# Kernel optimization log

Hardware: AMD Instinct MI355X
Metric: run time of the kernel (lower is better)

## Reference

```python
import jax, jax.numpy as jnp
import numpy as np
import math

B, T, D = 2, 2048, 2048
N_HEADS, N_KV_HEADS = 16, 4
HEAD_DIM = D // N_HEADS          # 128
N_GROUPS = N_HEADS // N_KV_HEADS # 4


def setup_inputs() -> dict:
    key = jax.random.key(0)
    k1, k2, k3, k4, k5 = jax.random.split(key, 5)
    x = jax.random.normal(k1, (B, T, D), dtype=jnp.float32)
    # RoPE table: [T, head_dim//2, 2] = (cos, sin)
    inv_freq = 1.0 / (10000.0 ** (np.arange(0, HEAD_DIM, 2, dtype=np.float32) / HEAD_DIM))
    ang = np.arange(T, dtype=np.float32)[:, None] * inv_freq[None, :]  # [T, hd/2]
    rope = jnp.asarray(np.stack([np.cos(ang), np.sin(ang)], axis=-1), dtype=jnp.float32)
    s = 0.02
    wq = s * jax.random.normal(k2, (N_HEADS * HEAD_DIM, D), dtype=jnp.float32)
    wk = s * jax.random.normal(k3, (N_KV_HEADS * HEAD_DIM, D), dtype=jnp.float32)
    wv = s * jax.random.normal(k4, (N_KV_HEADS * HEAD_DIM, D), dtype=jnp.float32)
    wo = s * jax.random.normal(k5, (D, D), dtype=jnp.float32)
    return {"x": x, "rope": rope, "wq": wq, "wk": wk, "wv": wv, "wo": wo}


def apply_rope(t, rope):
    # t: [B, H, T, hd]; rope: [T, hd/2, 2]
    d = t.shape[-1]
    t1, t2 = t[..., : d // 2], t[..., d // 2 :]
    cos = rope[..., 0][None, None]  # [1,1,T,hd/2]
    sin = rope[..., 1][None, None]
    return jnp.concatenate([t1 * cos - t2 * sin, t1 * sin + t2 * cos], axis=-1)


def reference(x, rope, wq, wk, wv, wo):
    b, t, c = x.shape
    q = (x @ wq.T).reshape(b, t, N_HEADS, HEAD_DIM).transpose(0, 2, 1, 3)
    k = (x @ wk.T).reshape(b, t, N_KV_HEADS, HEAD_DIM).transpose(0, 2, 1, 3)
    v = (x @ wv.T).reshape(b, t, N_KV_HEADS, HEAD_DIM).transpose(0, 2, 1, 3)
    q = apply_rope(q, rope)
    k = apply_rope(k, rope)
    k = jnp.repeat(k, N_GROUPS, axis=1)  # [B, H, T, hd]
    v = jnp.repeat(v, N_GROUPS, axis=1)
    scale = 1.0 / math.sqrt(HEAD_DIM)
    scores = jnp.einsum("bhqd,bhkd->bhqk", q, k) * scale
    causal = jnp.tril(jnp.ones((t, t), dtype=bool))
    scores = jnp.where(causal[None, None], scores, jnp.finfo(scores.dtype).min)
    attn = jax.nn.softmax(scores, axis=-1)
    y = jnp.einsum("bhqk,bhkd->bhqd", attn, v)
    y = y.transpose(0, 2, 1, 3).reshape(b, t, c)
    return y @ wo.T
```

## Files before the change

kernel.cpp:

```cpp
#include <hip/hip_runtime.h>

typedef unsigned short u16;
typedef float   f32x4  __attribute__((ext_vector_type(4)));
typedef short   short8 __attribute__((ext_vector_type(8)));
typedef __bf16  bf16x8 __attribute__((ext_vector_type(8)));
typedef float   float4v __attribute__((ext_vector_type(4)));
typedef unsigned short u16x4 __attribute__((ext_vector_type(4)));

static __device__ __forceinline__ u16 f2b(float f) {
  return __builtin_bit_cast(u16, (__bf16)f);
}
static __device__ __forceinline__ float b2f(u16 h) {
  union { unsigned u; float f; } v; v.u = ((unsigned)h) << 16;
  return v.f;
}
static __device__ __forceinline__ f32x4 mfma_bf16(short8 a, short8 b, f32x4 c) {
  return __builtin_amdgcn_mfma_f32_16x16x32_bf16(
      __builtin_bit_cast(bf16x8, a), __builtin_bit_cast(bf16x8, b), c, 0, 0, 0);
}
static __device__ __forceinline__ void gload_lds16(const u16* g, u16* l) {
  __builtin_amdgcn_global_load_lds(
      (const __attribute__((address_space(1))) unsigned int*)g,
      (__attribute__((address_space(3))) unsigned int*)l, 16, 0, 0);
}

#define BB 2
#define TT 2048
#define DD 2048
#define NH 16
#define NKVH 4
#define HD 128
#define MM (BB * TT)
#define QSTR 3072
#define QSCALE 0.08838834764831845f

#define N4_X   ((MM * DD) / 4)
#define N4_WQ  ((DD * DD) / 4)
#define N4_WKV ((NKVH * HD * DD) / 4)
#define N4_WO  ((DD * DD) / 4)
#define N4_TOT (N4_X + N4_WQ + 2 * N4_WKV + N4_WO)

__global__ __launch_bounds__(256) void cvt_all(const float* __restrict__ x,
                                               const float* __restrict__ wq,
                                               const float* __restrict__ wk,
                                               const float* __restrict__ wv,
                                               const float* __restrict__ wo,
                                               u16* __restrict__ xb,
                                               u16* __restrict__ wqkvb,
                                               u16* __restrict__ wob) {
  int stride = gridDim.x * blockDim.x;
  for (int i = blockIdx.x * blockDim.x + threadIdx.x; i < N4_TOT; i += stride) {
    const float4v* src;
    u16x4* dst;
    int off;
    if (i < N4_X) {
      src = (const float4v*)x; dst = (u16x4*)xb; off = i;
    } else if (i < N4_X + N4_WQ) {
      src = (const float4v*)wq; dst = (u16x4*)wqkvb; off = i - N4_X;
    } else if (i < N4_X + N4_WQ + N4_WKV) {
      src = (const float4v*)wk; dst = (u16x4*)wqkvb + N4_WQ; off = i - (N4_X + N4_WQ);
    } else if (i < N4_X + N4_WQ + 2 * N4_WKV) {
      src = (const float4v*)wv; dst = (u16x4*)wqkvb + N4_WQ + N4_WKV;
      off = i - (N4_X + N4_WQ + N4_WKV);
    } else {
      src = (const float4v*)wo; dst = (u16x4*)wob; off = i - (N4_X + N4_WQ + 2 * N4_WKV);
    }
    float4v v = src[off];
    u16x4 o;
    o[0] = f2b(v[0]); o[1] = f2b(v[1]); o[2] = f2b(v[2]); o[3] = f2b(v[3]);
    dst[off] = o;
  }
}

__global__ __launch_bounds__(256) void rope_k(u16* __restrict__ K,
                                              const float* __restrict__ rope) {
  int idx = blockIdx.x * 256 + threadIdx.x;
  int i  = idx & 63;
  int h  = (idx >> 6) & (NKVH - 1);
  int bt = idx >> 8;
  int t  = bt & (TT - 1);
  size_t base = (size_t)bt * QSTR + h * HD + i;
  float x1 = b2f(K[base]);
  float x2 = b2f(K[base + 64]);
  float c = rope[t * 128 + 2 * i];
  float s = rope[t * 128 + 2 * i + 1];
  K[base]      = f2b(x1 * c - x2 * s);
  K[base + 64] = f2b(x1 * s + x2 * c);
}

template <bool OUTBF>
__global__ __launch_bounds__(256) void gemm_bt(const u16* __restrict__ A,
                                               const u16* __restrict__ W,
                                               void* __restrict__ Cout,
                                               int M, int N, int K) {
  __shared__ __align__(16) u16 As[128 * 32];
  __shared__ __align__(16) u16 Ws[128 * 32];
  const int tid = threadIdx.x, lane = tid & 63, wid = tid >> 6;
  const int wr = wid >> 1, wc = wid & 1;
  const int gx = gridDim.x;
  const int lin = blockIdx.y * gx + blockIdx.x;
  const int cpx = (gx * gridDim.y) >> 3;
  const int swz = (lin & 7) * cpx + (lin >> 3);
  const int brow = (swz / gx) * 128, bcol = (swz % gx) * 128;
  const int l15 = lane & 15, lh = lane >> 4;

  const int c0 = wid * 64 + lane;
  const int c1 = c0 + 256;
  const u16* Ag0 = A + (size_t)(brow + (c0 >> 2)) * K + ((c0 & 3) << 3);
  const u16* Ag1 = A + (size_t)(brow + (c1 >> 2)) * K + ((c1 & 3) << 3);
  const u16* Wg0 = W + (size_t)(bcol + (c0 >> 2)) * K + ((c0 & 3) << 3);
  const u16* Wg1 = W + (size_t)(bcol + (c1 >> 2)) * K + ((c1 & 3) << 3);
  u16* lA0 = &As[(wid * 64) * 8];
  u16* lA1 = &As[(wid * 64 + 256) * 8];
  u16* lW0 = &Ws[(wid * 64) * 8];
  u16* lW1 = &Ws[(wid * 64 + 256) * 8];

  f32x4 acc[4][4];
#pragma unroll
  for (int m = 0; m < 4; ++m)
#pragma unroll
    for (int n = 0; n < 4; ++n) acc[m][n] = (f32x4)0.0f;

  for (int k0 = 0; k0 < K; k0 += 32) {
    __syncthreads();
    gload_lds16(Ag0 + k0, lA0);
    gload_lds16(Ag1 + k0, lA1);
    gload_lds16(Wg0 + k0, lW0);
    gload_lds16(Wg1 + k0, lW1);
    __syncthreads();
    short8 af[4], bfr[4];
#pragma unroll
    for (int m = 0; m < 4; ++m)
      af[m] = *(const short8*)&As[(wr * 64 + m * 16 + l15) * 32 + (lh << 3)];
#pragma unroll
    for (int n = 0; n < 4; ++n)
      bfr[n] = *(const short8*)&Ws[(wc * 64 + n * 16 + l15) * 32 + (lh << 3)];
#pragma unroll
    for (int m = 0; m < 4; ++m)
#pragma unroll
      for (int n = 0; n < 4; ++n)
        acc[m][n] = mfma_bf16(af[m], bfr[n], acc[m][n]);
  }

#pragma unroll
  for (int m = 0; m < 4; ++m)
#pragma unroll
    for (int n = 0; n < 4; ++n)
#pragma unroll
      for (int j = 0; j < 4; ++j) {
        int row = brow + wr * 64 + m * 16 + lh * 4 + j;
        int col = bcol + wc * 64 + n * 16 + l15;
        if (OUTBF)
          ((u16*)Cout)[(size_t)row * N + col] = f2b(acc[m][n][j]);
        else
          ((float*)Cout)[(size_t)row * N + col] = acc[m][n][j];
      }
}

#define QBLK 128
#define KVBLK 128

static __device__ __forceinline__ void attn_tile(
    const short8* qa, f32x4* o, f32x4& ol, float* mrow,
    int qrow0, int kv0,
    const u16* Ks, const unsigned* Vt32, u16* myP,
    int l15, int lh, short8 ones8) {
  if (kv0 > qrow0 + 15) return;

  f32x4 s[4];
#pragma unroll
  for (int nt = 0; nt < 4; ++nt) s[nt] = (f32x4)0.0f;
  __builtin_amdgcn_s_setprio(1);
#pragma unroll
  for (int nt = 0; nt < 4; ++nt)
#pragma unroll
    for (int kk = 0; kk < 4; ++kk) {
      short8 kb = *(const short8*)&Ks[(nt * 16 + l15) * 136 + kk * 32 + (lh << 3)];
      s[nt] = mfma_bf16(qa[kk], kb, s[nt]);
    }
  __builtin_amdgcn_s_setprio(0);

  const int qg = qrow0 + lh * 4;
#pragma unroll
  for (int j = 0; j < 4; ++j)
#pragma unroll
    for (int nt = 0; nt < 4; ++nt)
      if (kv0 + nt * 16 + l15 > qg + j) s[nt][j] = -1e30f;

  float mt[4];
#pragma unroll
  for (int j = 0; j < 4; ++j)
    mt[j] = fmaxf(fmaxf(s[0][j], s[1][j]), fmaxf(s[2][j], s[3][j]));
#pragma unroll
  for (int d = 1; d <= 8; d <<= 1)
#pragma unroll
    for (int j = 0; j < 4; ++j) mt[j] = fmaxf(mt[j], __shfl_xor(mt[j], d));

  float gmax = mt[0] - mrow[0];
#pragma unroll
  for (int j = 1; j < 4; ++j) gmax = fmaxf(gmax, mt[j] - mrow[j]);
  if (!__all(gmax <= 8.0f)) {
#pragma unroll
    for (int j = 0; j < 4; ++j) {
      float mn = fmaxf(mrow[j], mt[j]);
      float a = __expf(mrow[j] - mn);
      mrow[j] = mn;
      ol[j] *= a;
#pragma unroll
      for (int n = 0; n < 8; ++n) o[n][j] *= a;
    }
  }

  f32x4 p[4];
#pragma unroll
  for (int nt = 0; nt < 4; ++nt)
#pragma unroll
    for (int j = 0; j < 4; ++j) p[nt][j] = __expf(s[nt][j] - mrow[j]);

#pragma unroll
  for (int nt = 0; nt < 4; ++nt)
#pragma unroll
    for (int j = 0; j < 4; ++j)
      myP[(lh * 4 + j) * 72 + nt * 16 + l15] = f2b(p[nt][j]);

  __builtin_amdgcn_s_setprio(1);
#pragma unroll
  for (int c = 0; c < 2; ++c) {
    short8 pa = *(const short8*)&myP[l15 * 72 + c * 32 + (lh << 3)];
    ol = mfma_bf16(pa, ones8, ol);
#pragma unroll
    for (int nt2 = 0; nt2 < 8; ++nt2) {
      int d = nt2 * 16 + l15;
      int byteoff = (d * 144 + (c * 32 + lh * 8) * 2) ^ (((d >> 3) & 7) << 4);
      short8 vb = *(const short8*)((const char*)Vt32 + byteoff);
      o[nt2] = mfma_bf16(pa, vb, o[nt2]);
    }
  }
  __builtin_amdgcn_s_setprio(0);
}

__global__ __launch_bounds__(512) void attn_kernel(const u16* __restrict__ QKV,
                                                   const float* __restrict__ rope,
                                                   u16* __restrict__ Y) {
  __shared__ __align__(16) u16 Ks[2][64 * 136];
  __shared__ __align__(16) unsigned Vt32[2][128 * 36];
  __shared__ __align__(16) u16 Ps[8][16 * 72];

  const int tid = threadIdx.x, lane = tid & 63, wid = tid >> 6;
  const int l15 = lane & 15, lh = lane >> 4;
  const int bid = blockIdx.x;
  const int qpair = bid & 7;
  const int h = (bid >> 3) & 15;
  const int b = bid >> 7;
  const int kvh = h >> 2;
  const int qtA = qpair, qtB = 15 - qpair;
  const int rowA = qtA * QBLK + wid * 16;
  const int rowB = qtB * QBLK + wid * 16;

  const u16* Kb_ = QKV + (size_t)b * TT * QSTR + DD + kvh * HD;
  const u16* Vb_ = Kb_ + NKVH * HD;

  short8 ones8;
#pragma unroll
  for (int e = 0; e < 8; ++e) ones8[e] = (short)0x3F80;

  short8 qaA[4], qaB[4];
  {
    const u16* qA = QKV + (size_t)(b * TT + rowA + l15) * QSTR + h * HD + (lh << 3);
    const u16* qB = QKV + (size_t)(b * TT + rowB + l15) * QSTR + h * HD + (lh << 3);
#pragma unroll
    for (int kk = 0; kk < 4; ++kk) {
      qaA[kk] = *(const short8*)(qA + kk * 32);
      qaB[kk] = *(const short8*)(qB + kk * 32);
    }
  }
  {
    const float* rpA = rope + (size_t)(rowA + l15) * 128;
    const float* rpB = rope + (size_t)(rowB + l15) * 128;
#pragma unroll
    for (int kk = 0; kk < 2; ++kk)
#pragma unroll
      for (int e = 0; e < 8; ++e) {
        const int i2 = 2 * (kk * 32 + (lh << 3) + e);
        float c = rpA[i2], s = rpA[i2 + 1];
        float x1 = b2f((u16)qaA[kk][e]), x2 = b2f((u16)qaA[kk + 2][e]);
        qaA[kk][e]     = (short)f2b(QSCALE * (x1 * c - x2 * s));
        qaA[kk + 2][e] = (short)f2b(QSCALE * (x1 * s + x2 * c));
        float cb = rpB[i2], sb = rpB[i2 + 1];
        float y1 = b2f((u16)qaB[kk][e]), y2 = b2f((u16)qaB[kk + 2][e]);
        qaB[kk][e]     = (short)f2b(QSCALE * (y1 * cb - y2 * sb));
        qaB[kk + 2][e] = (short)f2b(QSCALE * (y1 * sb + y2 * cb));
      }
  }

  f32x4 oA[8], oB[8];
  f32x4 olA = (f32x4)0.0f, olB = (f32x4)0.0f;
  float mA[4], mB[4];
#pragma unroll
  for (int n = 0; n < 8; ++n) { oA[n] = (f32x4)0.0f; oB[n] = (f32x4)0.0f; }
#pragma unroll
  for (int j = 0; j < 4; ++j) { mA[j] = -1e30f; mB[j] = -1e30f; }

  const int kvend = (qtB + 1) * QBLK;

  short8 kreg[4], vreg[4];
  const int srow = tid >> 4;
  const int sc8 = (tid & 15) << 3;

  auto issue = [&](int kv0) {
    kreg[0] = *(const short8*)&Kb_[(size_t)(kv0 + srow) * QSTR + sc8];
    kreg[1] = *(const short8*)&Kb_[(size_t)(kv0 + 32 + srow) * QSTR + sc8];
    kreg[2] = *(const short8*)&Kb_[(size_t)(kv0 + 64 + srow) * QSTR + sc8];
    kreg[3] = *(const short8*)&Kb_[(size_t)(kv0 + 96 + srow) * QSTR + sc8];
    vreg[0] = *(const short8*)&Vb_[(size_t)(kv0 + 2 * srow) * QSTR + sc8];
    vreg[1] = *(const short8*)&Vb_[(size_t)(kv0 + 2 * srow + 1) * QSTR + sc8];
    vreg[2] = *(const short8*)&Vb_[(size_t)(kv0 + 64 + 2 * srow) * QSTR + sc8];
    vreg[3] = *(const short8*)&Vb_[(size_t)(kv0 + 64 + 2 * srow + 1) * QSTR + sc8];
  };

  issue(0);
  for (int kv0 = 0; kv0 < kvend; kv0 += KVBLK) {
    __syncthreads();
    *(short8*)&Ks[0][srow * 136 + sc8] = kreg[0];
    *(short8*)&Ks[0][(srow + 32) * 136 + sc8] = kreg[1];
    *(short8*)&Ks[1][srow * 136 + sc8] = kreg[2];
    *(short8*)&Ks[1][(srow + 32) * 136 + sc8] = kreg[3];
#pragma unroll
    for (int e = 0; e < 8; ++e) {
      int d = sc8 + e;
      unsigned pk0 = (unsigned)(u16)vreg[0][e] | ((unsigned)(u16)vreg[1][e] << 16);
      unsigned pk1 = (unsigned)(u16)vreg[2][e] | ((unsigned)(u16)vreg[3][e] << 16);
      int byteoff = (d * 144 + 4 * srow) ^ (((d >> 3) & 7) << 4);
      *(unsigned*)((char*)&Vt32[0][0] + byteoff) = pk0;
      *(unsigned*)((char*)&Vt32[1][0] + byteoff) = pk1;
    }
    __syncthreads();
    if (kv0 + KVBLK < kvend) issue(kv0 + KVBLK);

    attn_tile(qaA, oA, olA, mA, rowA, kv0,      &Ks[0][0], &Vt32[0][0], &Ps[wid][0], l15, lh, ones8);
    attn_tile(qaA, oA, olA, mA, rowA, kv0 + 64, &Ks[1][0], &Vt32[1][0], &Ps[wid][0], l15, lh, ones8);
    attn_tile(qaB, oB, olB, mB, rowB, kv0,      &Ks[0][0], &Vt32[0][0], &Ps[wid][0], l15, lh, ones8);
    attn_tile(qaB, oB, olB, mB, rowB, kv0 + 64, &Ks[1][0], &Vt32[1][0], &Ps[wid][0], l15, lh, ones8);
  }

  f32x4 invA, invB;
#pragma unroll
  for (int j = 0; j < 4; ++j) {
    invA[j] = __builtin_amdgcn_rcpf(olA[j]);
    invB[j] = __builtin_amdgcn_rcpf(olB[j]);
  }
#pragma unroll
  for (int nt = 0; nt < 8; ++nt)
#pragma unroll
    for (int j = 0; j < 4; ++j) {
      Y[(size_t)(b * TT + rowA + lh * 4 + j) * DD + h * HD + nt * 16 + l15] =
          f2b(oA[nt][j] * invA[j]);
      Y[(size_t)(b * TT + rowB + lh * 4 + j) * DD + h * HD + nt * 16 + l15] =
          f2b(oB[nt][j] * invB[j]);
    }
}

extern "C" void kernel_launch(void* const* d_in, const int* in_sizes, int n_in,
                              void* d_out, int out_size, void* d_ws, size_t ws_size,
                              hipStream_t stream) {
  const float* x    = (const float*)d_in[0];
  const float* rope = (const float*)d_in[1];
  const float* wq   = (const float*)d_in[2];
  const float* wk   = (const float*)d_in[3];
  const float* wv   = (const float*)d_in[4];
  const float* wo   = (const float*)d_in[5];
  float* out = (float*)d_out;

  char* ws = (char*)d_ws;
  u16* xb    = (u16*)ws; ws += (size_t)MM * DD * 2;
  u16* wqkvb = (u16*)ws; ws += (size_t)QSTR * DD * 2;
  u16* wob   = (u16*)ws; ws += (size_t)DD * DD * 2;
  u16* QKVb  = (u16*)ws; ws += (size_t)MM * QSTR * 2;
  u16* Yb    = (u16*)ws;

  cvt_all<<<2048, 256, 0, stream>>>(x, wq, wk, wv, wo, xb, wqkvb, wob);

  gemm_bt<true><<<dim3(QSTR / 128, MM / 128), 256, 0, stream>>>(xb, wqkvb, QKVb, MM, QSTR, DD);

  rope_k<<<(MM * NKVH * 64) / 256, 256, 0, stream>>>(QKVb + DD, rope);

  attn_kernel<<<BB * NH * (TT / QBLK / 2), 512, 0, stream>>>(QKVb, rope, Yb);

  gemm_bt<false><<<dim3(DD / 128, MM / 128), 256, 0, stream>>>(Yb, wob, out, MM, DD, DD);
}
```

Baseline: 226.6 us.

## Add large-tile double-buffered QKV projection GEMM with direct-to-LDS loads

Replaces the generic 128x128 GEMM for the fused QKV projection with a dedicated kernel. The new kernel uses 256x256 tiles with 512 threads, 64-wide K steps and double-buffered LDS filled by global-to-LDS loads. It uses XOR-swizzled shared-memory layout and staged MFMA phases with wave priority hints. The aim is more data reuse per block and overlap of loads with MFMA work. In exchange, the launch shrinks to 192 workgroups, fewer than the CU count, and LDS use rises to about 128KB per block.

```diff
diff --git a/kernel.cpp b/kernel.cpp
--- a/kernel.cpp
+++ b/kernel.cpp
@@ -88,6 +88,163 @@
   K[base + 64] = f2b(x1 * s + x2 * c);
 }
 
+__global__ __launch_bounds__(512, 2) void gemm_qkv(const u16* __restrict__ A,
+                                                   const u16* __restrict__ W,
+                                                   u16* __restrict__ C,
+                                                   int M, int N, int K) {
+  __shared__ __align__(16) u16 As[2][2][128 * 64];
+  __shared__ __align__(16) u16 Ws[2][2][128 * 64];
+
+  const int tid = threadIdx.x, lane = tid & 63, wid = tid >> 6;
+  const int wm = wid >> 2, wn = wid & 3;
+  const int l15 = lane & 15, lh = lane >> 4;
+
+  const int nwg = gridDim.x * gridDim.y;
+  const int lin = blockIdx.y * gridDim.x + blockIdx.x;
+  const int swz = (lin & 7) * (nwg >> 3) + (lin >> 3);
+  const int brow = (swz / gridDim.x) * 256, bcol = (swz % gridDim.x) * 256;
+
+  const int srp = wid * 8 + (lane >> 3);
+  const int gsw = ((lane & 7) ^ (lane >> 3)) << 3;
+  const u16* sa[2][2];
+  const u16* sw[2][2];
+#pragma unroll
+  for (int mh = 0; mh < 2; ++mh)
+#pragma unroll
+    for (int i = 0; i < 2; ++i) {
+      sa[mh][i] = A + (size_t)(brow + mh * 128 + i * 64 + srp) * K + gsw;
+      sw[mh][i] = W + (size_t)(bcol + mh * 128 + i * 64 + srp) * K + gsw;
+    }
+
+  f32x4 acc[8][4];
+#pragma unroll
+  for (int mi = 0; mi < 8; ++mi)
+#pragma unroll
+    for (int ni = 0; ni < 4; ++ni) acc[mi][ni] = (f32x4)0.0f;
+
+  const int nk = K >> 6;
+
+  auto issue = [&](int t, int p) {
+#pragma unroll
+    for (int mh = 0; mh < 2; ++mh)
+#pragma unroll
+      for (int i = 0; i < 2; ++i) {
+        gload_lds16(sa[mh][i] + t * 64, &As[p][mh][i * 4096 + wid * 512]);
+        gload_lds16(sw[mh][i] + t * 64, &Ws[p][mh][i * 4096 + wid * 512]);
+      }
+  };
+
+  issue(0, 0);
+  for (int t = 0; t < nk; ++t) {
+    const int p = t & 1;
+    if (t + 1 < nk) {
+      issue(t + 1, p ^ 1);
+      asm volatile("s_waitcnt vmcnt(8)" ::: "memory");
+    } else {
+      asm volatile("s_waitcnt vmcnt(0)" ::: "memory");
+    }
+    __builtin_amdgcn_sched_barrier(0);
+    __builtin_amdgcn_s_barrier();
+    __builtin_amdgcn_sched_barrier(0);
+
+    const u16* Ab = &As[p][wm][0];
+    const u16* Wb = &Ws[p][wn >> 1][0];
+    const int wrow = (wn & 1) * 64;
+
+    short8 af[4][2], bf[2][2];
+#pragma unroll
+    for (int mi = 0; mi < 4; ++mi)
+#pragma unroll
+      for (int ks = 0; ks < 2; ++ks) {
+        int rh = mi * 16 + l15;
+        af[mi][ks] = *(const short8*)&Ab[rh * 64 + (((ks * 4 + lh) ^ (rh & 7)) << 3)];
+      }
+#pragma unroll
+    for (int ni = 0; ni < 2; ++ni)
+#pragma unroll
+      for (int ks = 0; ks < 2; ++ks) {
+        int rh = wrow + ni * 16 + l15;
+        bf[ni][ks] = *(const short8*)&Wb[rh * 64 + (((ks * 4 + lh) ^ (rh & 7)) << 3)];
+      }
+    __builtin_amdgcn_s_setprio(1);
+#pragma unroll
+    for (int mi = 0; mi < 4; ++mi)
+#pragma unroll
+      for (int ni = 0; ni < 2; ++ni)
+#pragma unroll
+        for (int ks = 0; ks < 2; ++ks)
+          acc[mi][ni] = mfma_bf16(af[mi][ks], bf[ni][ks], acc[mi][ni]);
+    __builtin_amdgcn_s_setprio(0);
+    __builtin_amdgcn_s_barrier();
+#pragma unroll
+    for (int ni = 0; ni < 2; ++ni)
+#pragma unroll
+      for (int ks = 0; ks < 2; ++ks) {
+        int rh = wrow + (2 + ni) * 16 + l15;
+        bf[ni][ks] = *(const short8*)&Wb[rh * 64 + (((ks * 4 + lh) ^ (rh & 7)) << 3)];
+      }
+    __builtin_amdgcn_s_setprio(1);
+#pragma unroll
+    for (int mi = 0; mi < 4; ++mi)
+#pragma unroll
+      for (int ni = 0; ni < 2; ++ni)
+#pragma unroll
+        for (int ks = 0; ks < 2; ++ks)
+          acc[mi][2 + ni] = mfma_bf16(af[mi][ks], bf[ni][ks], acc[mi][2 + ni]);
+    __builtin_amdgcn_s_setprio(0);
+    __builtin_amdgcn_s_barrier();
+#pragma unroll
+    for (int mi = 0; mi < 4; ++mi)
+#pragma unroll
+      for (int ks = 0; ks < 2; ++ks) {
+        int rh = (4 + mi) * 16 + l15;
+        af[mi][ks] = *(const short8*)&Ab[rh * 64 + (((ks * 4 + lh) ^ (rh & 7)) << 3)];
+      }
+    __builtin_amdgcn_s_setprio(1);
+#pragma unroll
+    for (int mi = 0; mi < 4; ++mi)
+#pragma unroll
+      for (int ni = 0; ni < 2; ++ni)
+#pragma unroll
+        for (int ks = 0; ks < 2; ++ks)
+          acc[4 + mi][2 + ni] = mfma_bf16(af[mi][ks], bf[ni][ks], acc[4 + mi][2 + ni]);
+    __builtin_amdgcn_s_setprio(0);
+    __builtin_amdgcn_s_barrier();
+#pragma unroll
+    for (int ni = 0; ni < 2; ++ni)
+#pragma unroll
+      for (int ks = 0; ks < 2; ++ks) {
+        int rh = wrow + ni * 16 + l15;
+        bf[ni][ks] = *(const short8*)&Wb[rh * 64 + (((ks * 4 + lh) ^ (rh & 7)) << 3)];
+      }
+    __builtin_amdgcn_s_setprio(1);
+#pragma unroll
+    for (int mi = 0; mi < 4; ++mi)
+#pragma unroll
+      for (int ni = 0; ni < 2; ++ni)
+#pragma unroll
+        for (int ks = 0; ks < 2; ++ks)
+          acc[4 + mi][ni] = mfma_bf16(af[mi][ks], bf[ni][ks], acc[4 + mi][ni]);
+    __builtin_amdgcn_s_setprio(0);
+
+    asm volatile("s_waitcnt lgkmcnt(0)" ::: "memory");
+    __builtin_amdgcn_sched_barrier(0);
+    __builtin_amdgcn_s_barrier();
+    __builtin_amdgcn_sched_barrier(0);
+  }
+
+#pragma unroll
+  for (int mi = 0; mi < 8; ++mi)
+#pragma unroll
+    for (int ni = 0; ni < 4; ++ni)
+#pragma unroll
+      for (int j = 0; j < 4; ++j) {
+        int row = brow + wm * 128 + mi * 16 + lh * 4 + j;
+        int col = bcol + wn * 64 + ni * 16 + l15;
+        C[(size_t)row * N + col] = f2b(acc[mi][ni][j]);
+      }
+}
+
 template <bool OUTBF>
 __global__ __launch_bounds__(256) void gemm_bt(const u16* __restrict__ A,
                                                const u16* __restrict__ W,
@@ -380,7 +537,7 @@
 
   cvt_all<<<2048, 256, 0, stream>>>(x, wq, wk, wv, wo, xb, wqkvb, wob);
 
-  gemm_bt<true><<<dim3(QSTR / 128, MM / 128), 256, 0, stream>>>(xb, wqkvb, QKVb, MM, QSTR, DD);
+  gemm_qkv<<<dim3(QSTR / 256, MM / 256), 512, 0, stream>>>(xb, wqkvb, QKVb, MM, QSTR, DD);
 
   rope_k<<<(MM * NKVH * 64) / 256, 256, 0, stream>>>(QKVb + DD, rope);
 
```

New measurement: 227.0 us. No clear change (+0.2%).
